# Performance work log

Hardware: AMD Instinct MI355X
Metric: run time of the kernel (lower is better)

## Reference

```python
import jax, jax.numpy as jnp
import numpy as np

# Model dims (match init_kwargs)
B, S, H = 1, 2048, 1024
E = 16            # n_routed_experts
I = 768           # moe_intermediate_size
TOPK = 4          # num_experts_per_tok
G = 4             # n_group
TOPK_G = 2        # topk_group
SCALE = 2.5       # routed_scaling_factor
N_SHARED = 1      # n_shared_experts


def setup_inputs() -> dict:
    key = jax.random.key(0)
    ks = jax.random.split(key, 9)
    def rn(k, shape, scale=0.02):
        return jax.random.normal(k, shape, dtype=jnp.float32) * scale
    return dict(
        hidden_states=jax.random.normal(ks[0], (B, S, H), dtype=jnp.float32),
        gate_w=rn(ks[1], (E, H)),
        gate_bias=jax.random.normal(ks[2], (E,), dtype=jnp.float32) * 0.1,
        w1=rn(ks[3], (E, I, H)),   # gate_proj weights [out,in]
        w2=rn(ks[4], (E, H, I)),   # down_proj weights
        w3=rn(ks[5], (E, I, H)),   # up_proj weights
        ws1=rn(ks[6], (I * N_SHARED, H)),
        ws2=rn(ks[7], (H, I * N_SHARED)),
        ws3=rn(ks[8], (I * N_SHARED, H)),
    )


def _route(x, gate_w, gate_bias):
    """noaux_tc routing: sigmoid scores + bias, group top-k, top_k experts."""
    n = x.shape[0]
    logits = jnp.einsum('nh,eh->ne', x.astype(jnp.float32), gate_w)  # [N,E]
    scores = jax.nn.sigmoid(logits)
    sb = scores + gate_bias                                          # biased scores
    # group score = sum of top-2 biased scores in each group
    gs = sb.reshape(n, G, E // G)
    group_scores = jnp.sum(jax.lax.top_k(gs, 2)[0], axis=-1)         # [N,G]
    _, gidx = jax.lax.top_k(group_scores, TOPK_G)                    # [N,TOPK_G]
    gmask = jnp.sum(jax.nn.one_hot(gidx, G, dtype=sb.dtype), axis=1) # [N,G]
    emask = jnp.repeat(gmask, E // G, axis=-1)                       # [N,E]
    masked = jnp.where(emask > 0, sb, -jnp.inf)
    _, tidx = jax.lax.top_k(masked, TOPK)                            # [N,TOPK]
    w = jnp.take_along_axis(scores, tidx, axis=1)                    # unbiased weights
    w = w / (jnp.sum(w, axis=-1, keepdims=True) + 1e-20)             # norm_topk_prob
    return tidx, w * SCALE


def reference(hidden_states, gate_w, gate_bias, w1, w2, w3, ws1, ws2, ws3):
    b, s, h = hidden_states.shape
    x = hidden_states.reshape(-1, h)                                 # [N,H]
    tidx, tw = _route(x, gate_w, gate_bias)
    n = x.shape[0]
    # dense combine weights [N,E] (zero for unselected experts)
    combine = jnp.zeros((n, E), x.dtype).at[jnp.arange(n)[:, None], tidx].add(tw)
    # grouped SwiGLU experts (dense-over-experts reference form)
    g = jnp.einsum('nh,eih->nei', x, w1)
    u = jnp.einsum('nh,eih->nei', x, w3)
    hact = jax.nn.silu(g) * u * combine[:, :, None]
    y = jnp.einsum('nei,ehi->nh', hact, w2)
    # shared expert SwiGLU
    shared = jnp.einsum('ni,hi->nh', jax.nn.silu(x @ ws1.T) * (x @ ws3.T), ws2)
    return (y + shared).reshape(b, s, h)
```

## Files before the change

kernel.cpp:

```cpp
#include <hip/hip_runtime.h>
#include <hip/hip_bf16.h>
#include <math.h>

#define N_TOK 2048
#define H_DIM 1024
#define N_EXP 16
#define I_DIM 768
#define TOPK 4
#define SCALE 2.5f

#define GU_SLOTS 256
#define DN_SLOTS 192
#define GU_TAB (8 * GU_SLOTS)
#define DN_TAB (8 * DN_SLOTS)
#define GU_NY (I_DIM / 64)
#define DN_NY (H_DIM / 128)
#define MAX_GRP 832

typedef __attribute__((ext_vector_type(8))) short bf16x8;
typedef __attribute__((ext_vector_type(4))) float f32x4;

#define OFF_COUNTS   0
#define OFF_OFFSETS  128
#define OFF_WGU      256
#define OFF_WDN      (OFF_WGU + GU_TAB*4)
#define OFF_TOKIDS   (OFF_WDN + DN_TAB*4)
#define OFF_TOKW     (OFF_TOKIDS + N_EXP*N_TOK*4)
#define OFF_INV      (OFF_TOKW + N_EXP*N_TOK*4)
#define OFF_XB       (OFF_INV + N_TOK*TOPK*4)
#define OFF_HACT     (OFF_XB + (size_t)N_TOK*H_DIM*2)
#define OFF_YTMP     (OFF_HACT + (size_t)N_TOK*(TOPK+1)*I_DIM*2)

__device__ __forceinline__ ushort f2bf(float f) {
    union { __hip_bfloat16 h; ushort u; } cv;
    cv.h = __float2bfloat16(f);
    return cv.u;
}
__device__ __forceinline__ unsigned pack2(float lo, float hi) {
    return (unsigned)f2bf(lo) | ((unsigned)f2bf(hi) << 16);
}
__device__ __forceinline__ void async_copy16(const void* g, void* l) {
    __builtin_amdgcn_global_load_lds(
        (const __attribute__((address_space(1))) unsigned int*)g,
        (__attribute__((address_space(3))) unsigned int*)l, 16, 0, 0);
}

__launch_bounds__(256)
__global__ void k_route(const float* __restrict__ x, const float* __restrict__ gw,
                        const float* __restrict__ gb,
                        int* __restrict__ counts, int* __restrict__ tok_ids,
                        float* __restrict__ tok_w, ushort* __restrict__ xb,
                        int* __restrict__ inv) {
    __shared__ float lgs[4][N_EXP + 1];
    int tid = threadIdx.x;
    int wv = tid >> 6, lane = tid & 63;
    int e = lane & 15, ks = lane >> 4;
    int n = blockIdx.x * 4 + wv;

    const float* xr = x + (size_t)n * H_DIM + ks * 256;
    ushort* xbr = xb + (size_t)n * H_DIM + ks * 256;
    const float* wr = gw + (size_t)e * H_DIM + ks * 256;
    float a0 = 0.f, a1 = 0.f, a2 = 0.f, a3 = 0.f;
#pragma unroll 8
    for (int k = 0; k < 256; k += 4) {
        float4 xv = *(const float4*)(xr + k);
        float4 wvv = *(const float4*)(wr + k);
        a0 += xv.x * wvv.x;
        a1 += xv.y * wvv.y;
        a2 += xv.z * wvv.z;
        a3 += xv.w * wvv.w;
        if (e == 0) {
            uint2 p;
            p.x = pack2(xv.x, xv.y);
            p.y = pack2(xv.z, xv.w);
            *(uint2*)(xbr + k) = p;
        }
    }
    float acc = (a0 + a1) + (a2 + a3);
    acc += __shfl_xor(acc, 16);
    acc += __shfl_xor(acc, 32);
    if (lane < 16) lgs[wv][lane] = acc;
    __syncthreads();

    if (tid < 4) {
        int n2 = blockIdx.x * 4 + tid;
        float sc[N_EXP], sb[N_EXP];
        for (int ee = 0; ee < N_EXP; ee++) {
            float l = lgs[tid][ee];
            sc[ee] = 1.f / (1.f + expf(-l));
            sb[ee] = sc[ee] + gb[ee];
        }
        float gsc[4];
        for (int g = 0; g < 4; g++) {
            float m1 = -1e30f, m2 = -1e30f;
            for (int j = 0; j < 4; j++) {
                float v = sb[4 * g + j];
                if (v > m1) { m2 = m1; m1 = v; }
                else if (v > m2) m2 = v;
            }
            gsc[g] = m1 + m2;
        }
        int g1 = 0;
        for (int g = 1; g < 4; g++) if (gsc[g] > gsc[g1]) g1 = g;
        int g2 = -1;
        for (int g = 0; g < 4; g++) {
            if (g == g1) continue;
            if (g2 < 0 || gsc[g] > gsc[g2]) g2 = g;
        }
        bool allowed[N_EXP];
        for (int ee = 0; ee < N_EXP; ee++) {
            int grp = ee >> 2;
            allowed[ee] = (grp == g1) || (grp == g2);
        }
        int chosen[TOPK];
        float wsum = 0.f;
        for (int k = 0; k < TOPK; k++) {
            int best = -1;
            for (int ee = 0; ee < N_EXP; ee++) {
                if (!allowed[ee]) continue;
                if (best < 0 || sb[ee] > sb[best]) best = ee;
            }
            chosen[k] = best;
            allowed[best] = false;
            wsum += sc[best];
        }
        float inv_w = SCALE / (wsum + 1e-20f);
        for (int k = 0; k < TOPK; k++) {
            int ee = chosen[k];
            int p = atomicAdd(&counts[ee], 1);
            tok_ids[ee * N_TOK + p] = n2;
            tok_w[ee * N_TOK + p] = sc[ee] * inv_w;
            inv[n2 * TOPK + k] = (ee << 16) | p;
        }
    }
}

__global__ void k_scan(const int* __restrict__ counts, int* __restrict__ offsets,
                       int* __restrict__ wgu, int* __restrict__ wdn) {
    __shared__ int nmt_s[20], gpe_s[20];
    __shared__ int geb[20], deb[20];
    __shared__ int gmeta[MAX_GRP];
    __shared__ int gslot[MAX_GRP];
    __shared__ int ngu_s, ntot_s;
    int tid = threadIdx.x;
    for (int i = tid; i < GU_TAB; i += 256) wgu[i] = -1;
    for (int i = tid; i < DN_TAB; i += 256) wdn[i] = -1;
    if (tid < 17) {
        int c = (tid == 16) ? N_TOK : counts[tid];
        int nm = (c + 127) >> 7;
        nmt_s[tid] = nm;
        gpe_s[tid] = (nm + 3) >> 2;
    }
    __syncthreads();
    if (tid == 0) {
        int off = 0;
        for (int e = 0; e < N_EXP; e++) { offsets[e] = off; off += counts[e]; }
        offsets[N_EXP] = off;
        int g = 0, d = 0;
        for (int e = 0; e <= N_EXP; e++) {
            geb[e] = g; g += GU_NY * gpe_s[e];
            deb[e] = d; d += DN_NY * gpe_s[e];
        }
        geb[N_EXP + 1] = g; deb[N_EXP + 1] = d;
        ngu_s = g; ntot_s = g + d;
    }
    __syncthreads();
    int ngu = ngu_s, ntot = ntot_s;
    for (int g = tid; g < ntot; g += 256) {
        bool gu = g < ngu;
        int r = gu ? g : g - ngu;
        const int* eb = gu ? geb : deb;
        int e = 0;
        while (eb[e + 1] <= r) e++;
        int rem = r - eb[e];
        int gp = gpe_s[e];
        int y = rem / gp, mc = rem - y * gp;
        int m0t = mc * 4;
        int size = nmt_s[e] - m0t; if (size > 4) size = 4;
        gmeta[g] = e | (m0t << 5) | (y << 9) | (size << 24);
    }
    __syncthreads();
    if (tid < 8) {
        int s = 0;
        for (int g = tid; g < ngu; g += 8) { gslot[g] = s; s += (gmeta[g] >> 24); }
    } else if (tid < 16) {
        int c = tid - 8, s = 0;
        for (int g = ngu + c; g < ntot; g += 8) { gslot[g] = s; s += (gmeta[g] >> 24); }
    }
    __syncthreads();
    int k = tid & 3;
    for (int g = tid >> 2; g < ntot; g += 64) {
        int p = gmeta[g];
        int size = (p >> 24);
        if (k >= size) continue;
        int desc = (p & 0x1FFF) + (k << 5);
        bool gu = g < ngu;
        int r = gu ? g : g - ngu;
        int idx = (r & 7) + 8 * (gslot[g] + k);
        if (gu) wgu[idx] = desc; else wdn[idx] = desc;
    }
}

__launch_bounds__(256, 3)
__global__ void k_gateup(const ushort* __restrict__ xb, const float* __restrict__ w1,
                         const float* __restrict__ w3, const float* __restrict__ ws1,
                         const float* __restrict__ ws3, const int* __restrict__ counts,
                         const int* __restrict__ offsets, const int* __restrict__ wgu,
                         const int* __restrict__ tok_ids, const float* __restrict__ tok_w,
                         ushort* __restrict__ hact) {
    int desc = wgu[blockIdx.x];
    if (desc < 0) return;
    int e = desc & 31;
    int m0 = ((desc >> 5) & 15) * 128;
    int i0 = ((desc >> 9) & 15) * 64;
    int Me = (e == N_EXP) ? N_TOK : counts[e];
    const float* W1 = (e == N_EXP) ? ws1 : w1 + (size_t)e * I_DIM * H_DIM;
    const float* W3 = (e == N_EXP) ? ws3 : w3 + (size_t)e * I_DIM * H_DIM;
    int base = offsets[e];

    __shared__ ushort As[2][128][64];
    __shared__ ushort Bs[128][64];
    __shared__ float tws[128];

    int tid = threadIdx.x;
    int wv = tid >> 6, lane = tid & 63;
    int wm = wv >> 1, wn = wv & 1;
    int seg = lane & 7, rsub = lane >> 3;
    int gch = (seg ^ rsub) * 8;

    if (tid < 128) {
        int r = m0 + tid;
        tws[tid] = (e == N_EXP) ? 1.f : ((r < Me) ? tok_w[e * N_TOK + r] : 0.f);
    }

    const ushort* aptr[4];
#pragma unroll
    for (int j = 0; j < 4; j++) {
        int gr = m0 + wv * 32 + j * 8 + rsub;
        int tok = (e == N_EXP) ? gr : ((gr < Me) ? tok_ids[e * N_TOK + gr] : 0);
        aptr[j] = xb + (size_t)tok * H_DIM + gch;
    }
    const float* bptrf[4];
#pragma unroll
    for (int j = 0; j < 4; j++) {
        int r = wv * 32 + j * 8 + rsub;
        const float* W = (r < 64) ? (W1 + (size_t)(i0 + r) * H_DIM)
                                  : (W3 + (size_t)(i0 + r - 64) * H_DIM);
        bptrf[j] = W + gch;
    }

    int quad = lane >> 4, lr = lane & 15, rx = lr & 7;
    f32x4 acc[4][4] = {};

    const int NK = H_DIM / 64;
    float4 bv0[4], bv1[4];
#pragma unroll
    for (int j = 0; j < 4; j++) async_copy16(aptr[j], &As[0][wv * 32 + j * 8][0]);
#pragma unroll
    for (int j = 0; j < 4; j++) {
        bv0[j] = *(const float4*)(bptrf[j]);
        bv1[j] = *(const float4*)(bptrf[j] + 4);
    }
#pragma unroll
    for (int j = 0; j < 4; j++) {
        uint4 p;
        p.x = pack2(bv0[j].x, bv0[j].y);
        p.y = pack2(bv0[j].z, bv0[j].w);
        p.z = pack2(bv1[j].x, bv1[j].y);
        p.w = pack2(bv1[j].z, bv1[j].w);
        *(uint4*)&Bs[wv * 32 + j * 8 + rsub][seg * 8] = p;
    }

    int c = 0;
    for (int k = 0; k < NK; k++) {
        __syncthreads();
        if (k + 1 < NK) {
#pragma unroll
            for (int j = 0; j < 4; j++)
                async_copy16(aptr[j] + (k + 1) * 64, &As[c ^ 1][wv * 32 + j * 8][0]);
#pragma unroll
            for (int j = 0; j < 4; j++) {
                bv0[j] = *(const float4*)(bptrf[j] + (k + 1) * 64);
                bv1[j] = *(const float4*)(bptrf[j] + (k + 1) * 64 + 4);
            }
        }
#pragma unroll
        for (int ks = 0; ks < 2; ks++) {
            int co = ((ks * 4 + quad) ^ rx) * 8;
            bf16x8 af[4], bf[4];
#pragma unroll
            for (int mi = 0; mi < 4; mi++)
                af[mi] = *(const bf16x8*)&As[c][wm * 64 + mi * 16 + lr][co];
#pragma unroll
            for (int ni = 0; ni < 4; ni++) {
                int brow = ((ni & 2) ? 64 : 0) + wn * 32 + (ni & 1) * 16;
                bf[ni] = *(const bf16x8*)&Bs[brow + lr][co];
            }
#pragma unroll
            for (int mi = 0; mi < 4; mi++)
#pragma unroll
                for (int ni = 0; ni < 4; ni++)
                    acc[mi][ni] = __builtin_amdgcn_mfma_f32_16x16x32_bf16(
                        af[mi], bf[ni], acc[mi][ni], 0, 0, 0);
        }
        __syncthreads();
        if (k + 1 < NK) {
#pragma unroll
            for (int j = 0; j < 4; j++) {
                uint4 p;
                p.x = pack2(bv0[j].x, bv0[j].y);
                p.y = pack2(bv0[j].z, bv0[j].w);
                p.z = pack2(bv1[j].x, bv1[j].y);
                p.w = pack2(bv1[j].z, bv1[j].w);
                *(uint4*)&Bs[wv * 32 + j * 8 + rsub][seg * 8] = p;
            }
        }
        c ^= 1;
    }

#pragma unroll
    for (int mi = 0; mi < 4; mi++) {
#pragma unroll
        for (int ni = 0; ni < 2; ni++) {
            f32x4 g = acc[mi][ni];
            f32x4 u = acc[mi][ni + 2];
#pragma unroll
            for (int rg = 0; rg < 4; rg++) {
                int ml = wm * 64 + mi * 16 + quad * 4 + rg;
                int row = m0 + ml;
                if (row < Me) {
                    float gg = g[rg], uu = u[rg];
                    float act = (gg / (1.f + expf(-gg))) * uu * tws[ml];
                    hact[(size_t)(base + row) * I_DIM + i0 + wn * 32 + ni * 16 + lr]
                        = f2bf(act);
                }
            }
        }
    }
}

__launch_bounds__(256, 3)
__global__ void k_down(const ushort* __restrict__ hact, const float* __restrict__ w2,
                       const float* __restrict__ ws2, const int* __restrict__ counts,
                       const int* __restrict__ offsets, const int* __restrict__ wdn,
                       float* __restrict__ ytmp) {
    int desc = wdn[blockIdx.x];
    if (desc < 0) return;
    int e = desc & 31;
    int m0 = ((desc >> 5) & 15) * 128;
    int h0 = ((desc >> 9) & 15) * 128;
    int Me = (e == N_EXP) ? N_TOK : counts[e];
    const float* W2 = (e == N_EXP) ? ws2 : w2 + (size_t)e * H_DIM * I_DIM;
    int base = offsets[e];

    __shared__ ushort As[2][128][64];
    __shared__ ushort Bs[128][64];

    int tid = threadIdx.x;
    int wv = tid >> 6, lane = tid & 63;
    int wm = wv >> 1, wn = wv & 1;
    int seg = lane & 7, rsub = lane >> 3;
    int gch = (seg ^ rsub) * 8;

    const ushort* aptr[4];
#pragma unroll
    for (int j = 0; j < 4; j++) {
        int row = wv * 32 + j * 8 + rsub;
        aptr[j] = hact + (size_t)(base + m0 + row) * I_DIM + gch;
    }
    const float* bptrf[4];
#pragma unroll
    for (int j = 0; j < 4; j++) {
        int r = wv * 32 + j * 8 + rsub;
        bptrf[j] = W2 + (size_t)(h0 + r) * I_DIM + gch;
    }

    int quad = lane >> 4, lr = lane & 15, rx = lr & 7;
    f32x4 acc[4][4] = {};

    const int NK = I_DIM / 64;
    float4 bv0[4], bv1[4];
#pragma unroll
    for (int j = 0; j < 4; j++) async_copy16(aptr[j], &As[0][wv * 32 + j * 8][0]);
#pragma unroll
    for (int j = 0; j < 4; j++) {
        bv0[j] = *(const float4*)(bptrf[j]);
        bv1[j] = *(const float4*)(bptrf[j] + 4);
    }
#pragma unroll
    for (int j = 0; j < 4; j++) {
        uint4 p;
        p.x = pack2(bv0[j].x, bv0[j].y);
        p.y = pack2(bv0[j].z, bv0[j].w);
        p.z = pack2(bv1[j].x, bv1[j].y);
        p.w = pack2(bv1[j].z, bv1[j].w);
        *(uint4*)&Bs[wv * 32 + j * 8 + rsub][seg * 8] = p;
    }

    int c = 0;
    for (int k = 0; k < NK; k++) {
        __syncthreads();
        if (k + 1 < NK) {
#pragma unroll
            for (int j = 0; j < 4; j++)
                async_copy16(aptr[j] + (k + 1) * 64, &As[c ^ 1][wv * 32 + j * 8][0]);
#pragma unroll
            for (int j = 0; j < 4; j++) {
                bv0[j] = *(const float4*)(bptrf[j] + (k + 1) * 64);
                bv1[j] = *(const float4*)(bptrf[j] + (k + 1) * 64 + 4);
            }
        }
#pragma unroll
        for (int ks = 0; ks < 2; ks++) {
            int co = ((ks * 4 + quad) ^ rx) * 8;
            bf16x8 af[4], bf[4];
#pragma unroll
            for (int mi = 0; mi < 4; mi++)
                af[mi] = *(const bf16x8*)&As[c][wm * 64 + mi * 16 + lr][co];
#pragma unroll
            for (int ni = 0; ni < 4; ni++)
                bf[ni] = *(const bf16x8*)&Bs[wn * 64 + ni * 16 + lr][co];
#pragma unroll
            for (int mi = 0; mi < 4; mi++)
#pragma unroll
                for (int ni = 0; ni < 4; ni++)
                    acc[mi][ni] = __builtin_amdgcn_mfma_f32_16x16x32_bf16(
                        af[mi], bf[ni], acc[mi][ni], 0, 0, 0);
        }
        __syncthreads();
        if (k + 1 < NK) {
#pragma unroll
            for (int j = 0; j < 4; j++) {
                uint4 p;
                p.x = pack2(bv0[j].x, bv0[j].y);
                p.y = pack2(bv0[j].z, bv0[j].w);
                p.z = pack2(bv1[j].x, bv1[j].y);
                p.w = pack2(bv1[j].z, bv1[j].w);
                *(uint4*)&Bs[wv * 32 + j * 8 + rsub][seg * 8] = p;
            }
        }
        c ^= 1;
    }

#pragma unroll
    for (int mi = 0; mi < 4; mi++) {
#pragma unroll
        for (int ni = 0; ni < 4; ni++) {
#pragma unroll
            for (int rg = 0; rg < 4; rg++) {
                int ml = wm * 64 + mi * 16 + quad * 4 + rg;
                int row = m0 + ml;
                if (row < Me) {
                    ytmp[(size_t)(base + row) * H_DIM + h0 + wn * 64 + ni * 16 + lr]
                        = acc[mi][ni][rg];
                }
            }
        }
    }
}

__launch_bounds__(256)
__global__ void k_reduce(const float* __restrict__ ytmp, const int* __restrict__ inv,
                         const int* __restrict__ offsets, float* __restrict__ out) {
    int t = blockIdx.x, tid = threadIdx.x;
    const float4* yt = (const float4*)ytmp;
    float4 s = yt[(size_t)(offsets[N_EXP] + t) * (H_DIM / 4) + tid];
#pragma unroll
    for (int k = 0; k < TOPK; k++) {
        int v = inv[t * TOPK + k];
        int slot = offsets[v >> 16] + (v & 0xFFFF);
        float4 a = yt[(size_t)slot * (H_DIM / 4) + tid];
        s.x += a.x; s.y += a.y; s.z += a.z; s.w += a.w;
    }
    ((float4*)out)[(size_t)t * (H_DIM / 4) + tid] = s;
}

extern "C" void kernel_launch(void* const* d_in, const int* in_sizes, int n_in,
                              void* d_out, int out_size, void* d_ws, size_t ws_size,
                              hipStream_t stream) {
    const float* x   = (const float*)d_in[0];
    const float* gw  = (const float*)d_in[1];
    const float* gb  = (const float*)d_in[2];
    const float* w1  = (const float*)d_in[3];
    const float* w2  = (const float*)d_in[4];
    const float* w3  = (const float*)d_in[5];
    const float* ws1 = (const float*)d_in[6];
    const float* ws2 = (const float*)d_in[7];
    const float* ws3 = (const float*)d_in[8];
    float* out = (float*)d_out;

    char* wsb = (char*)d_ws;
    int* counts   = (int*)(wsb + OFF_COUNTS);
    int* offsets  = (int*)(wsb + OFF_OFFSETS);
    int* wgu      = (int*)(wsb + OFF_WGU);
    int* wdn      = (int*)(wsb + OFF_WDN);
    int* tok_ids  = (int*)(wsb + OFF_TOKIDS);
    float* tok_w  = (float*)(wsb + OFF_TOKW);
    int* inv      = (int*)(wsb + OFF_INV);
    ushort* xb    = (ushort*)(wsb + OFF_XB);
    ushort* hact  = (ushort*)(wsb + OFF_HACT);
    float* ytmp   = (float*)(wsb + OFF_YTMP);

    hipMemsetAsync(wsb, 0, 128, stream);

    k_route<<<N_TOK / 4, 256, 0, stream>>>(x, gw, gb, counts, tok_ids, tok_w, xb, inv);
    k_scan<<<1, 256, 0, stream>>>(counts, offsets, wgu, wdn);
    k_gateup<<<GU_TAB, 256, 0, stream>>>(xb, w1, w3, ws1, ws3, counts, offsets,
                                         wgu, tok_ids, tok_w, hact);
    k_down<<<DN_TAB, 256, 0, stream>>>(hact, w2, ws2, counts, offsets, wdn, ytmp);
    k_reduce<<<N_TOK, 256, 0, stream>>>(ytmp, inv, offsets, out);
}
```

Measured before the change: 358.5 us.

## Load expert weights directly into MFMA B fragments, bypassing shared memory

```diff
diff --git a/kernel.cpp b/kernel.cpp
--- a/kernel.cpp
+++ b/kernel.cpp
@@ -43,6 +43,14 @@
     __builtin_amdgcn_global_load_lds(
         (const __attribute__((address_space(1))) unsigned int*)g,
         (__attribute__((address_space(3))) unsigned int*)l, 16, 0, 0);
+}
+__device__ __forceinline__ bf16x8 cvt_frag(float4 a, float4 b) {
+    union { bf16x8 v; unsigned u[4]; } cc;
+    cc.u[0] = pack2(a.x, a.y);
+    cc.u[1] = pack2(a.z, a.w);
+    cc.u[2] = pack2(b.x, b.y);
+    cc.u[3] = pack2(b.z, b.w);
+    return cc.v;
 }
 
 __launch_bounds__(256)
@@ -219,7 +227,6 @@
     int base = offsets[e];
 
     __shared__ ushort As[2][128][64];
-    __shared__ ushort Bs[128][64];
     __shared__ float tws[128];
 
     int tid = threadIdx.x;
@@ -240,80 +247,91 @@
         int tok = (e == N_EXP) ? gr : ((gr < Me) ? tok_ids[e * N_TOK + gr] : 0);
         aptr[j] = xb + (size_t)tok * H_DIM + gch;
     }
-    const float* bptrf[4];
-#pragma unroll
-    for (int j = 0; j < 4; j++) {
-        int r = wv * 32 + j * 8 + rsub;
-        const float* W = (r < 64) ? (W1 + (size_t)(i0 + r) * H_DIM)
-                                  : (W3 + (size_t)(i0 + r - 64) * H_DIM);
-        bptrf[j] = W + gch;
-    }
 
     int quad = lane >> 4, lr = lane & 15, rx = lr & 7;
+
+    const float* bp[4];
+#pragma unroll
+    for (int ni = 0; ni < 4; ni++) {
+        int r = i0 + wn * 32 + (ni & 1) * 16 + lr;
+        const float* W = (ni < 2) ? W1 : W3;
+        bp[ni] = W + (size_t)r * H_DIM + quad * 8;
+    }
+
     f32x4 acc[4][4] = {};
+    bf16x8 F[2][4];
+    float4 nb[8];
 
     const int NK = H_DIM / 64;
-    float4 bv0[4], bv1[4];
 #pragma unroll
     for (int j = 0; j < 4; j++) async_copy16(aptr[j], &As[0][wv * 32 + j * 8][0]);
 #pragma unroll
-    for (int j = 0; j < 4; j++) {
-        bv0[j] = *(const float4*)(bptrf[j]);
-        bv1[j] = *(const float4*)(bptrf[j] + 4);
-    }
-#pragma unroll
-    for (int j = 0; j < 4; j++) {
-        uint4 p;
-        p.x = pack2(bv0[j].x, bv0[j].y);
-        p.y = pack2(bv0[j].z, bv0[j].w);
-        p.z = pack2(bv1[j].x, bv1[j].y);
-        p.w = pack2(bv1[j].z, bv1[j].w);
-        *(uint4*)&Bs[wv * 32 + j * 8 + rsub][seg * 8] = p;
-    }
+    for (int ni = 0; ni < 4; ni++) {
+        nb[2 * ni]     = *(const float4*)(bp[ni]);
+        nb[2 * ni + 1] = *(const float4*)(bp[ni] + 4);
+    }
+#pragma unroll
+    for (int ni = 0; ni < 4; ni++) F[0][ni] = cvt_frag(nb[2 * ni], nb[2 * ni + 1]);
+#pragma unroll
+    for (int ni = 0; ni < 4; ni++) {
+        nb[2 * ni]     = *(const float4*)(bp[ni] + 32);
+        nb[2 * ni + 1] = *(const float4*)(bp[ni] + 36);
+    }
+#pragma unroll
+    for (int ni = 0; ni < 4; ni++) F[1][ni] = cvt_frag(nb[2 * ni], nb[2 * ni + 1]);
 
     int c = 0;
     for (int k = 0; k < NK; k++) {
         __syncthreads();
+        int nxt = (k + 1) * 64;
         if (k + 1 < NK) {
 #pragma unroll
             for (int j = 0; j < 4; j++)
-                async_copy16(aptr[j] + (k + 1) * 64, &As[c ^ 1][wv * 32 + j * 8][0]);
-#pragma unroll
-            for (int j = 0; j < 4; j++) {
-                bv0[j] = *(const float4*)(bptrf[j] + (k + 1) * 64);
-                bv1[j] = *(const float4*)(bptrf[j] + (k + 1) * 64 + 4);
-            }
-        }
-#pragma unroll
-        for (int ks = 0; ks < 2; ks++) {
-            int co = ((ks * 4 + quad) ^ rx) * 8;
-            bf16x8 af[4], bf[4];
+                async_copy16(aptr[j] + nxt, &As[c ^ 1][wv * 32 + j * 8][0]);
+#pragma unroll
+            for (int ni = 0; ni < 4; ni++) {
+                nb[2 * ni]     = *(const float4*)(bp[ni] + nxt);
+                nb[2 * ni + 1] = *(const float4*)(bp[ni] + nxt + 4);
+            }
+        }
+        {
+            int co = ((0 * 4 + quad) ^ rx) * 8;
+            bf16x8 af[4];
 #pragma unroll
             for (int mi = 0; mi < 4; mi++)
                 af[mi] = *(const bf16x8*)&As[c][wm * 64 + mi * 16 + lr][co];
-#pragma unroll
-            for (int ni = 0; ni < 4; ni++) {
-                int brow = ((ni & 2) ? 64 : 0) + wn * 32 + (ni & 1) * 16;
-                bf[ni] = *(const bf16x8*)&Bs[brow + lr][co];
-            }
 #pragma unroll
             for (int mi = 0; mi < 4; mi++)
 #pragma unroll
                 for (int ni = 0; ni < 4; ni++)
                     acc[mi][ni] = __builtin_amdgcn_mfma_f32_16x16x32_bf16(
-                        af[mi], bf[ni], acc[mi][ni], 0, 0, 0);
-        }
-        __syncthreads();
+                        af[mi], F[0][ni], acc[mi][ni], 0, 0, 0);
+        }
         if (k + 1 < NK) {
 #pragma unroll
-            for (int j = 0; j < 4; j++) {
-                uint4 p;
-                p.x = pack2(bv0[j].x, bv0[j].y);
-                p.y = pack2(bv0[j].z, bv0[j].w);
-                p.z = pack2(bv1[j].x, bv1[j].y);
-                p.w = pack2(bv1[j].z, bv1[j].w);
-                *(uint4*)&Bs[wv * 32 + j * 8 + rsub][seg * 8] = p;
-            }
+            for (int ni = 0; ni < 4; ni++) F[0][ni] = cvt_frag(nb[2 * ni], nb[2 * ni + 1]);
+#pragma unroll
+            for (int ni = 0; ni < 4; ni++) {
+                nb[2 * ni]     = *(const float4*)(bp[ni] + nxt + 32);
+                nb[2 * ni + 1] = *(const float4*)(bp[ni] + nxt + 36);
+            }
+        }
+        {
+            int co = ((1 * 4 + quad) ^ rx) * 8;
+            bf16x8 af[4];
+#pragma unroll
+            for (int mi = 0; mi < 4; mi++)
+                af[mi] = *(const bf16x8*)&As[c][wm * 64 + mi * 16 + lr][co];
+#pragma unroll
+            for (int mi = 0; mi < 4; mi++)
+#pragma unroll
+                for (int ni = 0; ni < 4; ni++)
+                    acc[mi][ni] = __builtin_amdgcn_mfma_f32_16x16x32_bf16(
+                        af[mi], F[1][ni], acc[mi][ni], 0, 0, 0);
+        }
+        if (k + 1 < NK) {
+#pragma unroll
+            for (int ni = 0; ni < 4; ni++) F[1][ni] = cvt_frag(nb[2 * ni], nb[2 * ni + 1]);
         }
         c ^= 1;
     }
@@ -354,7 +372,6 @@
     int base = offsets[e];
 
     __shared__ ushort As[2][128][64];
-    __shared__ ushort Bs[128][64];
 
     int tid = threadIdx.x;
     int wv = tid >> 6, lane = tid & 63;
@@ -368,76 +385,90 @@
         int row = wv * 32 + j * 8 + rsub;
         aptr[j] = hact + (size_t)(base + m0 + row) * I_DIM + gch;
     }
-    const float* bptrf[4];
-#pragma unroll
-    for (int j = 0; j < 4; j++) {
-        int r = wv * 32 + j * 8 + rsub;
-        bptrf[j] = W2 + (size_t)(h0 + r) * I_DIM + gch;
-    }
 
     int quad = lane >> 4, lr = lane & 15, rx = lr & 7;
+
+    const float* bp[4];
+#pragma unroll
+    for (int ni = 0; ni < 4; ni++) {
+        int r = h0 + wn * 64 + ni * 16 + lr;
+        bp[ni] = W2 + (size_t)r * I_DIM + quad * 8;
+    }
+
     f32x4 acc[4][4] = {};
+    bf16x8 F[2][4];
+    float4 nb[8];
 
     const int NK = I_DIM / 64;
-    float4 bv0[4], bv1[4];
 #pragma unroll
     for (int j = 0; j < 4; j++) async_copy16(aptr[j], &As[0][wv * 32 + j * 8][0]);
 #pragma unroll
-    for (int j = 0; j < 4; j++) {
-        bv0[j] = *(const float4*)(bptrf[j]);
-        bv1[j] = *(const float4*)(bptrf[j] + 4);
-    }
-#pragma unroll
-    for (int j = 0; j < 4; j++) {
-        uint4 p;
-        p.x = pack2(bv0[j].x, bv0[j].y);
-        p.y = pack2(bv0[j].z, bv0[j].w);
-        p.z = pack2(bv1[j].x, bv1[j].y);
-        p.w = pack2(bv1[j].z, bv1[j].w);
-        *(uint4*)&Bs[wv * 32 + j * 8 + rsub][seg * 8] = p;
-    }
+    for (int ni = 0; ni < 4; ni++) {
+        nb[2 * ni]     = *(const float4*)(bp[ni]);
+        nb[2 * ni + 1] = *(const float4*)(bp[ni] + 4);
+    }
+#pragma unroll
+    for (int ni = 0; ni < 4; ni++) F[0][ni] = cvt_frag(nb[2 * ni], nb[2 * ni + 1]);
+#pragma unroll
+    for (int ni = 0; ni < 4; ni++) {
+        nb[2 * ni]     = *(const float4*)(bp[ni] + 32);
+        nb[2 * ni + 1] = *(const float4*)(bp[ni] + 36);
+    }
+#pragma unroll
+    for (int ni = 0; ni < 4; ni++) F[1][ni] = cvt_frag(nb[2 * ni], nb[2 * ni + 1]);
 
     int c = 0;
     for (int k = 0; k < NK; k++) {
         __syncthreads();
+        int nxt = (k + 1) * 64;
         if (k + 1 < NK) {
 #pragma unroll
             for (int j = 0; j < 4; j++)
-                async_copy16(aptr[j] + (k + 1) * 64, &As[c ^ 1][wv * 32 + j * 8][0]);
-#pragma unroll
-            for (int j = 0; j < 4; j++) {
-                bv0[j] = *(const float4*)(bptrf[j] + (k + 1) * 64);
-                bv1[j] = *(const float4*)(bptrf[j] + (k + 1) * 64 + 4);
-            }
-        }
-#pragma unroll
-        for (int ks = 0; ks < 2; ks++) {
-            int co = ((ks * 4 + quad) ^ rx) * 8;
-            bf16x8 af[4], bf[4];
+                async_copy16(aptr[j] + nxt, &As[c ^ 1][wv * 32 + j * 8][0]);
+#pragma unroll
+            for (int ni = 0; ni < 4; ni++) {
+                nb[2 * ni]     = *(const float4*)(bp[ni] + nxt);
+                nb[2 * ni + 1] = *(const float4*)(bp[ni] + nxt + 4);
+            }
+        }
+        {
+            int co = ((0 * 4 + quad) ^ rx) * 8;
+            bf16x8 af[4];
 #pragma unroll
             for (int mi = 0; mi < 4; mi++)
                 af[mi] = *(const bf16x8*)&As[c][wm * 64 + mi * 16 + lr][co];
-#pragma unroll
-            for (int ni = 0; ni < 4; ni++)
-                bf[ni] = *(const bf16x8*)&Bs[wn * 64 + ni * 16 + lr][co];
 #pragma unroll
             for (int mi = 0; mi < 4; mi++)
 #pragma unroll
                 for (int ni = 0; ni < 4; ni++)
                     acc[mi][ni] = __builtin_amdgcn_mfma_f32_16x16x32_bf16(
-                        af[mi], bf[ni], acc[mi][ni], 0, 0, 0);
-        }
-        __syncthreads();
+                        af[mi], F[0][ni], acc[mi][ni], 0, 0, 0);
+        }
         if (k + 1 < NK) {
 #pragma unroll
-            for (int j = 0; j < 4; j++) {
-                uint4 p;
-                p.x = pack2(bv0[j].x, bv0[j].y);
-                p.y = pack2(bv0[j].z, bv0[j].w);
-                p.z = pack2(bv1[j].x, bv1[j].y);
-                p.w = pack2(bv1[j].z, bv1[j].w);
-                *(uint4*)&Bs[wv * 32 + j * 8 + rsub][seg * 8] = p;
-            }
+            for (int ni = 0; ni < 4; ni++) F[0][ni] = cvt_frag(nb[2 * ni], nb[2 * ni + 1]);
+#pragma unroll
+            for (int ni = 0; ni < 4; ni++) {
+                nb[2 * ni]     = *(const float4*)(bp[ni] + nxt + 32);
+                nb[2 * ni + 1] = *(const float4*)(bp[ni] + nxt + 36);
+            }
+        }
+        {
+            int co = ((1 * 4 + quad) ^ rx) * 8;
+            bf16x8 af[4];
+#pragma unroll
+            for (int mi = 0; mi < 4; mi++)
+                af[mi] = *(const bf16x8*)&As[c][wm * 64 + mi * 16 + lr][co];
+#pragma unroll
+            for (int mi = 0; mi < 4; mi++)
+#pragma unroll
+                for (int ni = 0; ni < 4; ni++)
+                    acc[mi][ni] = __builtin_amdgcn_mfma_f32_16x16x32_bf16(
+                        af[mi], F[1][ni], acc[mi][ni], 0, 0, 0);
+        }
+        if (k + 1 < NK) {
+#pragma unroll
+            for (int ni = 0; ni < 4; ni++) F[1][ni] = cvt_frag(nb[2 * ni], nb[2 * ni + 1]);
         }
         c ^= 1;
     }
```

Result: slower. 520.5 us (+45.2%).

## Use 8-wave blocks with triple-buffered A tiles in MoE GEMM kernels

Applied to the files above, without the earlier changes.

```diff
diff --git a/kernel.cpp b/kernel.cpp
--- a/kernel.cpp
+++ b/kernel.cpp
@@ -201,7 +201,7 @@
     }
 }
 
-__launch_bounds__(256, 3)
+__launch_bounds__(512, 4)
 __global__ void k_gateup(const ushort* __restrict__ xb, const float* __restrict__ w1,
                          const float* __restrict__ w3, const float* __restrict__ ws1,
                          const float* __restrict__ ws3, const int* __restrict__ counts,
@@ -218,13 +218,13 @@
     const float* W3 = (e == N_EXP) ? ws3 : w3 + (size_t)e * I_DIM * H_DIM;
     int base = offsets[e];
 
-    __shared__ ushort As[2][128][64];
+    __shared__ ushort As[3][128][64];
     __shared__ ushort Bs[128][64];
     __shared__ float tws[128];
 
     int tid = threadIdx.x;
     int wv = tid >> 6, lane = tid & 63;
-    int wm = wv >> 1, wn = wv & 1;
+    int wm = wv >> 2, wn = wv & 3;
     int seg = lane & 7, rsub = lane >> 3;
     int gch = (seg ^ rsub) * 8;
 
@@ -233,113 +233,117 @@
         tws[tid] = (e == N_EXP) ? 1.f : ((r < Me) ? tok_w[e * N_TOK + r] : 0.f);
     }
 
-    const ushort* aptr[4];
-#pragma unroll
-    for (int j = 0; j < 4; j++) {
-        int gr = m0 + wv * 32 + j * 8 + rsub;
+    const ushort* aptr[2];
+#pragma unroll
+    for (int j = 0; j < 2; j++) {
+        int gr = m0 + wv * 16 + j * 8 + rsub;
         int tok = (e == N_EXP) ? gr : ((gr < Me) ? tok_ids[e * N_TOK + gr] : 0);
         aptr[j] = xb + (size_t)tok * H_DIM + gch;
     }
-    const float* bptrf[4];
-#pragma unroll
-    for (int j = 0; j < 4; j++) {
-        int r = wv * 32 + j * 8 + rsub;
+    const float* bptrf[2];
+#pragma unroll
+    for (int j = 0; j < 2; j++) {
+        int r = wv * 16 + j * 8 + rsub;
         const float* W = (r < 64) ? (W1 + (size_t)(i0 + r) * H_DIM)
                                   : (W3 + (size_t)(i0 + r - 64) * H_DIM);
         bptrf[j] = W + gch;
     }
 
     int quad = lane >> 4, lr = lane & 15, rx = lr & 7;
-    f32x4 acc[4][4] = {};
+    f32x4 acc[4][2] = {};
 
     const int NK = H_DIM / 64;
-    float4 bv0[4], bv1[4];
-#pragma unroll
-    for (int j = 0; j < 4; j++) async_copy16(aptr[j], &As[0][wv * 32 + j * 8][0]);
-#pragma unroll
-    for (int j = 0; j < 4; j++) {
+    float4 bv0[2], bv1[2];
+
+#pragma unroll
+    for (int j = 0; j < 2; j++) async_copy16(aptr[j], &As[0][wv * 16 + j * 8][0]);
+#pragma unroll
+    for (int j = 0; j < 2; j++) async_copy16(aptr[j] + 64, &As[1][wv * 16 + j * 8][0]);
+#pragma unroll
+    for (int j = 0; j < 2; j++) {
         bv0[j] = *(const float4*)(bptrf[j]);
         bv1[j] = *(const float4*)(bptrf[j] + 4);
     }
 #pragma unroll
-    for (int j = 0; j < 4; j++) {
+    for (int j = 0; j < 2; j++) {
         uint4 p;
         p.x = pack2(bv0[j].x, bv0[j].y);
         p.y = pack2(bv0[j].z, bv0[j].w);
         p.z = pack2(bv1[j].x, bv1[j].y);
         p.w = pack2(bv1[j].z, bv1[j].w);
-        *(uint4*)&Bs[wv * 32 + j * 8 + rsub][seg * 8] = p;
-    }
-
-    int c = 0;
+        *(uint4*)&Bs[wv * 16 + j * 8 + rsub][seg * 8] = p;
+    }
+    asm volatile("s_waitcnt lgkmcnt(0)" ::: "memory");
+    __builtin_amdgcn_s_barrier();
+    __builtin_amdgcn_sched_barrier(0);
+
     for (int k = 0; k < NK; k++) {
-        __syncthreads();
+        int cr = k % 3;
         if (k + 1 < NK) {
 #pragma unroll
-            for (int j = 0; j < 4; j++)
-                async_copy16(aptr[j] + (k + 1) * 64, &As[c ^ 1][wv * 32 + j * 8][0]);
-#pragma unroll
-            for (int j = 0; j < 4; j++) {
+            for (int j = 0; j < 2; j++) {
                 bv0[j] = *(const float4*)(bptrf[j] + (k + 1) * 64);
                 bv1[j] = *(const float4*)(bptrf[j] + (k + 1) * 64 + 4);
             }
         }
+        __builtin_amdgcn_sched_barrier(0);
+        if (k + 2 < NK) {
+            int cw = (k + 2) % 3;
+#pragma unroll
+            for (int j = 0; j < 2; j++)
+                async_copy16(aptr[j] + (k + 2) * 64, &As[cw][wv * 16 + j * 8][0]);
+        }
 #pragma unroll
         for (int ks = 0; ks < 2; ks++) {
             int co = ((ks * 4 + quad) ^ rx) * 8;
-            bf16x8 af[4], bf[4];
+            bf16x8 af[4];
 #pragma unroll
             for (int mi = 0; mi < 4; mi++)
-                af[mi] = *(const bf16x8*)&As[c][wm * 64 + mi * 16 + lr][co];
-#pragma unroll
-            for (int ni = 0; ni < 4; ni++) {
-                int brow = ((ni & 2) ? 64 : 0) + wn * 32 + (ni & 1) * 16;
-                bf[ni] = *(const bf16x8*)&Bs[brow + lr][co];
-            }
-#pragma unroll
-            for (int mi = 0; mi < 4; mi++)
-#pragma unroll
-                for (int ni = 0; ni < 4; ni++)
-                    acc[mi][ni] = __builtin_amdgcn_mfma_f32_16x16x32_bf16(
-                        af[mi], bf[ni], acc[mi][ni], 0, 0, 0);
-        }
-        __syncthreads();
+                af[mi] = *(const bf16x8*)&As[cr][wm * 64 + mi * 16 + lr][co];
+            bf16x8 b0 = *(const bf16x8*)&Bs[wn * 16 + lr][co];
+            bf16x8 b1 = *(const bf16x8*)&Bs[64 + wn * 16 + lr][co];
+#pragma unroll
+            for (int mi = 0; mi < 4; mi++) {
+                acc[mi][0] = __builtin_amdgcn_mfma_f32_16x16x32_bf16(af[mi], b0, acc[mi][0], 0, 0, 0);
+                acc[mi][1] = __builtin_amdgcn_mfma_f32_16x16x32_bf16(af[mi], b1, acc[mi][1], 0, 0, 0);
+            }
+        }
+        __builtin_amdgcn_s_barrier();
+        __builtin_amdgcn_sched_barrier(0);
         if (k + 1 < NK) {
 #pragma unroll
-            for (int j = 0; j < 4; j++) {
+            for (int j = 0; j < 2; j++) {
                 uint4 p;
                 p.x = pack2(bv0[j].x, bv0[j].y);
                 p.y = pack2(bv0[j].z, bv0[j].w);
                 p.z = pack2(bv1[j].x, bv1[j].y);
                 p.w = pack2(bv1[j].z, bv1[j].w);
-                *(uint4*)&Bs[wv * 32 + j * 8 + rsub][seg * 8] = p;
-            }
-        }
-        c ^= 1;
+                *(uint4*)&Bs[wv * 16 + j * 8 + rsub][seg * 8] = p;
+            }
+        }
+        asm volatile("s_waitcnt lgkmcnt(0)" ::: "memory");
+        __builtin_amdgcn_s_barrier();
+        __builtin_amdgcn_sched_barrier(0);
     }
 
 #pragma unroll
     for (int mi = 0; mi < 4; mi++) {
-#pragma unroll
-        for (int ni = 0; ni < 2; ni++) {
-            f32x4 g = acc[mi][ni];
-            f32x4 u = acc[mi][ni + 2];
-#pragma unroll
-            for (int rg = 0; rg < 4; rg++) {
-                int ml = wm * 64 + mi * 16 + quad * 4 + rg;
-                int row = m0 + ml;
-                if (row < Me) {
-                    float gg = g[rg], uu = u[rg];
-                    float act = (gg / (1.f + expf(-gg))) * uu * tws[ml];
-                    hact[(size_t)(base + row) * I_DIM + i0 + wn * 32 + ni * 16 + lr]
-                        = f2bf(act);
-                }
-            }
-        }
-    }
-}
-
-__launch_bounds__(256, 3)
+        f32x4 g = acc[mi][0];
+        f32x4 u = acc[mi][1];
+#pragma unroll
+        for (int rg = 0; rg < 4; rg++) {
+            int ml = wm * 64 + mi * 16 + quad * 4 + rg;
+            int row = m0 + ml;
+            if (row < Me) {
+                float gg = g[rg], uu = u[rg];
+                float act = (gg / (1.f + expf(-gg))) * uu * tws[ml];
+                hact[(size_t)(base + row) * I_DIM + i0 + wn * 16 + lr] = f2bf(act);
+            }
+        }
+    }
+}
+
+__launch_bounds__(512, 4)
 __global__ void k_down(const ushort* __restrict__ hact, const float* __restrict__ w2,
                        const float* __restrict__ ws2, const int* __restrict__ counts,
                        const int* __restrict__ offsets, const int* __restrict__ wdn,
@@ -353,105 +357,114 @@
     const float* W2 = (e == N_EXP) ? ws2 : w2 + (size_t)e * H_DIM * I_DIM;
     int base = offsets[e];
 
-    __shared__ ushort As[2][128][64];
+    __shared__ ushort As[3][128][64];
     __shared__ ushort Bs[128][64];
 
     int tid = threadIdx.x;
     int wv = tid >> 6, lane = tid & 63;
-    int wm = wv >> 1, wn = wv & 1;
+    int wm = wv >> 2, wn = wv & 3;
     int seg = lane & 7, rsub = lane >> 3;
     int gch = (seg ^ rsub) * 8;
 
-    const ushort* aptr[4];
-#pragma unroll
-    for (int j = 0; j < 4; j++) {
-        int row = wv * 32 + j * 8 + rsub;
+    const ushort* aptr[2];
+#pragma unroll
+    for (int j = 0; j < 2; j++) {
+        int row = wv * 16 + j * 8 + rsub;
         aptr[j] = hact + (size_t)(base + m0 + row) * I_DIM + gch;
     }
-    const float* bptrf[4];
-#pragma unroll
-    for (int j = 0; j < 4; j++) {
-        int r = wv * 32 + j * 8 + rsub;
+    const float* bptrf[2];
+#pragma unroll
+    for (int j = 0; j < 2; j++) {
+        int r = wv * 16 + j * 8 + rsub;
         bptrf[j] = W2 + (size_t)(h0 + r) * I_DIM + gch;
     }
 
     int quad = lane >> 4, lr = lane & 15, rx = lr & 7;
-    f32x4 acc[4][4] = {};
+    f32x4 acc[4][2] = {};
 
     const int NK = I_DIM / 64;
-    float4 bv0[4], bv1[4];
-#pragma unroll
-    for (int j = 0; j < 4; j++) async_copy16(aptr[j], &As[0][wv * 32 + j * 8][0]);
-#pragma unroll
-    for (int j = 0; j < 4; j++) {
+    float4 bv0[2], bv1[2];
+#pragma unroll
+    for (int j = 0; j < 2; j++) async_copy16(aptr[j], &As[0][wv * 16 + j * 8][0]);
+#pragma unroll
+    for (int j = 0; j < 2; j++) async_copy16(aptr[j] + 64, &As[1][wv * 16 + j * 8][0]);
+#pragma unroll
+    for (int j = 0; j < 2; j++) {
         bv0[j] = *(const float4*)(bptrf[j]);
         bv1[j] = *(const float4*)(bptrf[j] + 4);
     }
 #pragma unroll
-    for (int j = 0; j < 4; j++) {
+    for (int j = 0; j < 2; j++) {
         uint4 p;
         p.x = pack2(bv0[j].x, bv0[j].y);
         p.y = pack2(bv0[j].z, bv0[j].w);
         p.z = pack2(bv1[j].x, bv1[j].y);
         p.w = pack2(bv1[j].z, bv1[j].w);
-        *(uint4*)&Bs[wv * 32 + j * 8 + rsub][seg * 8] = p;
-    }
-
-    int c = 0;
+        *(uint4*)&Bs[wv * 16 + j * 8 + rsub][seg * 8] = p;
+    }
+    asm volatile("s_waitcnt lgkmcnt(0)" ::: "memory");
+    __builtin_amdgcn_s_barrier();
+    __builtin_amdgcn_sched_barrier(0);
+
     for (int k = 0; k < NK; k++) {
-        __syncthreads();
+        int cr = k % 3;
         if (k + 1 < NK) {
 #pragma unroll
-            for (int j = 0; j < 4; j++)
-                async_copy16(aptr[j] + (k + 1) * 64, &As[c ^ 1][wv * 32 + j * 8][0]);
-#pragma unroll
-            for (int j = 0; j < 4; j++) {
+            for (int j = 0; j < 2; j++) {
                 bv0[j] = *(const float4*)(bptrf[j] + (k + 1) * 64);
                 bv1[j] = *(const float4*)(bptrf[j] + (k + 1) * 64 + 4);
             }
         }
+        __builtin_amdgcn_sched_barrier(0);
+        if (k + 2 < NK) {
+            int cw = (k + 2) % 3;
+#pragma unroll
+            for (int j = 0; j < 2; j++)
+                async_copy16(aptr[j] + (k + 2) * 64, &As[cw][wv * 16 + j * 8][0]);
+        }
 #pragma unroll
         for (int ks = 0; ks < 2; ks++) {
             int co = ((ks * 4 + quad) ^ rx) * 8;
-            bf16x8 af[4], bf[4];
+            bf16x8 af[4];
 #pragma unroll
             for (int mi = 0; mi < 4; mi++)
-                af[mi] = *(const bf16x8*)&As[c][wm * 64 + mi * 16 + lr][co];
-#pragma unroll
-            for (int ni = 0; ni < 4; ni++)
-                bf[ni] = *(const bf16x8*)&Bs[wn * 64 + ni * 16 + lr][co];
-#pragma unroll
-            for (int mi = 0; mi < 4; mi++)
-#pragma unroll
-                for (int ni = 0; ni < 4; ni++)
-                    acc[mi][ni] = __builtin_amdgcn_mfma_f32_16x16x32_bf16(
-                        af[mi], bf[ni], acc[mi][ni], 0, 0, 0);
-        }
-        __syncthreads();
+                af[mi] = *(const bf16x8*)&As[cr][wm * 64 + mi * 16 + lr][co];
+            bf16x8 b0 = *(const bf16x8*)&Bs[wn * 32 + lr][co];
+            bf16x8 b1 = *(const bf16x8*)&Bs[wn * 32 + 16 + lr][co];
+#pragma unroll
+            for (int mi = 0; mi < 4; mi++) {
+                acc[mi][0] = __builtin_amdgcn_mfma_f32_16x16x32_bf16(af[mi], b0, acc[mi][0], 0, 0, 0);
+                acc[mi][1] = __builtin_amdgcn_mfma_f32_16x16x32_bf16(af[mi], b1, acc[mi][1], 0, 0, 0);
+            }
+        }
+        __builtin_amdgcn_s_barrier();
+        __builtin_amdgcn_sched_barrier(0);
         if (k + 1 < NK) {
 #pragma unroll
-            for (int j = 0; j < 4; j++) {
+            for (int j = 0; j < 2; j++) {
                 uint4 p;
                 p.x = pack2(bv0[j].x, bv0[j].y);
                 p.y = pack2(bv0[j].z, bv0[j].w);
                 p.z = pack2(bv1[j].x, bv1[j].y);
                 p.w = pack2(bv1[j].z, bv1[j].w);
-                *(uint4*)&Bs[wv * 32 + j * 8 + rsub][seg * 8] = p;
-            }
-        }
-        c ^= 1;
+                *(uint4*)&Bs[wv * 16 + j * 8 + rsub][seg * 8] = p;
+            }
+        }
+        asm volatile("s_waitcnt lgkmcnt(0)" ::: "memory");
+        __builtin_amdgcn_s_barrier();
+        __builtin_amdgcn_sched_barrier(0);
     }
 
 #pragma unroll
     for (int mi = 0; mi < 4; mi++) {
 #pragma unroll
-        for (int ni = 0; ni < 4; ni++) {
+        for (int ni = 0; ni < 2; ni++) {
 #pragma unroll
             for (int rg = 0; rg < 4; rg++) {
                 int ml = wm * 64 + mi * 16 + quad * 4 + rg;
                 int row = m0 + ml;
                 if (row < Me) {
-                    ytmp[(size_t)(base + row) * H_DIM + h0 + wn * 64 + ni * 16 + lr]
+                    ytmp[(size_t)(base + row) * H_DIM + h0 + wn * 32 + ni * 16 + lr]
                         = acc[mi][ni][rg];
                 }
             }
@@ -505,8 +518,8 @@
 
     k_route<<<N_TOK / 4, 256, 0, stream>>>(x, gw, gb, counts, tok_ids, tok_w, xb, inv);
     k_scan<<<1, 256, 0, stream>>>(counts, offsets, wgu, wdn);
-    k_gateup<<<GU_TAB, 256, 0, stream>>>(xb, w1, w3, ws1, ws3, counts, offsets,
+    k_gateup<<<GU_TAB, 512, 0, stream>>>(xb, w1, w3, ws1, ws3, counts, offsets,
                                          wgu, tok_ids, tok_w, hact);
-    k_down<<<DN_TAB, 256, 0, stream>>>(hact, w2, ws2, counts, offsets, wdn, ytmp);
+    k_down<<<DN_TAB, 512, 0, stream>>>(hact, w2, ws2, counts, offsets, wdn, ytmp);
     k_reduce<<<N_TOK, 256, 0, stream>>>(ytmp, inv, offsets, out);
 }
```

Result: slower. 366.5 us (+2.2%).
